# Kernel optimization log

Measured on AMD Instinct MI355X. Metric: run time of the kernel, lower is better.

Reference implementation:

```python
import jax, jax.numpy as jnp
import numpy as np

B, W, H = 128, 512, 512


def setup_inputs() -> dict:
    key = jax.random.key(0)
    ks = jax.random.split(key, 10)
    s = 1.0 / np.sqrt(H)
    return {
        "g": jax.random.normal(ks[0], (B, H), jnp.float32),
        "c_g": jax.random.normal(ks[1], (B, H), jnp.float32),
        "h": jax.random.normal(ks[2], (B, W, H), jnp.float32),
        "c": jax.random.normal(ks[3], (B, W, H), jnp.float32),
        "W_w": jax.random.normal(ks[4], (2 * H, H), jnp.float32) * s,
        "w_w": jax.random.normal(ks[5], (H, H), jnp.float32) * s,
        "U_w": jax.random.normal(ks[6], (2 * H, H), jnp.float32) * s,
        "U_b": jax.random.normal(ks[7], (2 * H,), jnp.float32) * s,
        "u_w": jax.random.normal(ks[8], (H, H), jnp.float32) * s,
        "u_b": jax.random.normal(ks[9], (H,), jnp.float32) * s,
    }


def reference(g, c_g, h, c, W_w, w_w, U_w, U_b, u_w, u_b):
    hid = w_w.shape[0]
    # attn_pooling: mean over word dim -> [B, H]
    h_avg = jnp.mean(h, axis=-2)
    # gates f, o: [B, H] each
    fo = jax.nn.sigmoid(g @ W_w.T + h_avg @ U_w.T + U_b)
    f, o = fo[..., :hid], fo[..., hid:]
    # per-word forget weights, softmax over word dim: [B, W, H]
    f_w = jax.nn.sigmoid((g @ w_w.T)[..., None, :] + h @ u_w.T + u_b)
    f_w = jax.nn.softmax(f_w, axis=-2)
    new_c = f * c_g + jnp.sum(c * f_w, axis=-2)
    new_g = o * jnp.tanh(new_c)
    return new_g, new_c
```

## Files before the change

kernel.cpp:

```cpp
#include <hip/hip_runtime.h>
#include <stdint.h>

#define BB 128
#define WW 512
#define HH 512
#define TILE 128
#define BK 64

typedef __attribute__((ext_vector_type(8))) short bf16x8;
typedef __attribute__((ext_vector_type(4))) float f32x4;

__device__ __forceinline__ float bf2f(unsigned short u) {
  union { unsigned int i; float f; } v;
  v.i = ((unsigned int)u) << 16;
  return v.f;
}
__device__ __forceinline__ unsigned int pack_bf2(float lo, float hi) {
  union { float f; unsigned int u; } a, b;
  a.f = lo; b.f = hi;
  return (a.u >> 16) | (b.u & 0xFFFF0000u);
}
__device__ __forceinline__ float dot4f(float4 u, const float* gp) {
  return u.x * gp[0] + u.y * gp[1] + u.z * gp[2] + u.w * gp[3];
}

__global__ __launch_bounds__(256) void k1_mfma(
    const float* __restrict__ g, const float* __restrict__ W_w,
    const float* __restrict__ w_w,
    float* __restrict__ gw, float* __restrict__ gfo) {
  __shared__ __align__(16) unsigned short As[TILE * BK];
  __shared__ __align__(16) unsigned short Bs[TILE * BK];
  const int nc = blockIdx.x;
  const int t = threadIdx.x;
  const int lane = t & 63, wave = t >> 6;
  const int wm = wave >> 1, wn = wave & 1;
  const int l15 = lane & 15, quad = lane >> 4;

  const float* wsrc = (nc < 4) ? (w_w + (size_t)nc * TILE * HH)
                               : (W_w + (size_t)(nc - 4) * TILE * HH);

  const f32x4 zero = {0.f, 0.f, 0.f, 0.f};
  f32x4 acc[4][4];
#pragma unroll
  for (int i = 0; i < 4; ++i)
#pragma unroll
    for (int j = 0; j < 4; ++j) acc[i][j] = zero;

  const int srow = t >> 3;
  const int scol = (t & 7) * 8;

  for (int kt = 0; kt < 8; ++kt) {
    const int k0 = kt * BK;
#pragma unroll
    for (int p = 0; p < 4; ++p) {
      const int row = p * 32 + srow;
      const float4* ap = (const float4*)(g    + (size_t)row * HH + k0 + scol);
      const float4* bp = (const float4*)(wsrc + (size_t)row * HH + k0 + scol);
      float4 a0 = ap[0], a1 = ap[1], b0 = bp[0], b1 = bp[1];
      uint4 av, bv;
      av.x = pack_bf2(a0.x, a0.y); av.y = pack_bf2(a0.z, a0.w);
      av.z = pack_bf2(a1.x, a1.y); av.w = pack_bf2(a1.z, a1.w);
      bv.x = pack_bf2(b0.x, b0.y); bv.y = pack_bf2(b0.z, b0.w);
      bv.z = pack_bf2(b1.x, b1.y); bv.w = pack_bf2(b1.z, b1.w);
      *(uint4*)(As + row * BK + scol) = av;
      *(uint4*)(Bs + row * BK + scol) = bv;
    }
    __syncthreads();
#pragma unroll
    for (int ks = 0; ks < 2; ++ks) {
      bf16x8 af[4], bg[4];
#pragma unroll
      for (int i = 0; i < 4; ++i)
        af[i] = *(const bf16x8*)(As + (wm * 64 + i * 16 + l15) * BK + ks * 32 + quad * 8);
#pragma unroll
      for (int j = 0; j < 4; ++j)
        bg[j] = *(const bf16x8*)(Bs + (wn * 64 + j * 16 + l15) * BK + ks * 32 + quad * 8);
#pragma unroll
      for (int i = 0; i < 4; ++i)
#pragma unroll
        for (int j = 0; j < 4; ++j)
          acc[i][j] = __builtin_amdgcn_mfma_f32_16x16x32_bf16(af[i], bg[j], acc[i][j], 0, 0, 0);
    }
    __syncthreads();
  }

#pragma unroll
  for (int j = 0; j < 4; ++j) {
    const int nl = wn * 64 + j * 16 + l15;
#pragma unroll
    for (int i = 0; i < 4; ++i) {
#pragma unroll
      for (int r = 0; r < 4; ++r) {
        const int b = wm * 64 + i * 16 + quad * 4 + r;
        const float v = acc[i][j][r];
        if (nc < 4) gw[(size_t)b * HH + nc * TILE + nl] = v;
        else        gfo[(size_t)b * 2 * HH + (nc - 4) * TILE + nl] = v;
      }
    }
  }
}

__global__ __launch_bounds__(256) void k2_main(
    const float* __restrict__ h, const float* __restrict__ c,
    const float* __restrict__ u_w, const float* __restrict__ u_b,
    const float* __restrict__ gw,
    float* __restrict__ hsumP, float* __restrict__ denP, float* __restrict__ numP) {
  __shared__ __align__(16) unsigned short As[TILE * BK];
  __shared__ __align__(16) unsigned short Bs[TILE * BK];
  __shared__ float colred[4][64];
  __shared__ float redD[2][TILE];
  __shared__ float redN[2][TILE];

  const int bid = blockIdx.x;
  const int b  = bid >> 4;
  const int wc = (bid >> 2) & 3;
  const int nc = bid & 3;
  const int t = threadIdx.x;
  const int lane = t & 63, wave = t >> 6;
  const int wm = wave >> 1, wn = wave & 1;
  const int l15 = lane & 15, quad = lane >> 4;

  const size_t hbase = ((size_t)b * WW + (size_t)wc * TILE) * HH;
  const size_t ubase = (size_t)nc * TILE * HH;

  const f32x4 zero = {0.f, 0.f, 0.f, 0.f};
  f32x4 acc[4][4];
#pragma unroll
  for (int i = 0; i < 4; ++i)
#pragma unroll
    for (int j = 0; j < 4; ++j) acc[i][j] = zero;

  const int srow = t >> 3;
  const int scol = (t & 7) * 8;

  for (int kt = 0; kt < 8; ++kt) {
    const int k0 = kt * BK;
#pragma unroll
    for (int p = 0; p < 4; ++p) {
      const int row = p * 32 + srow;
      const float4* ap = (const float4*)(h   + hbase + (size_t)row * HH + k0 + scol);
      const float4* bp = (const float4*)(u_w + ubase + (size_t)row * HH + k0 + scol);
      float4 a0 = ap[0], a1 = ap[1], b0 = bp[0], b1 = bp[1];
      uint4 av, bv;
      av.x = pack_bf2(a0.x, a0.y); av.y = pack_bf2(a0.z, a0.w);
      av.z = pack_bf2(a1.x, a1.y); av.w = pack_bf2(a1.z, a1.w);
      bv.x = pack_bf2(b0.x, b0.y); bv.y = pack_bf2(b0.z, b0.w);
      bv.z = pack_bf2(b1.x, b1.y); bv.w = pack_bf2(b1.z, b1.w);
      *(uint4*)(As + row * BK + scol) = av;
      *(uint4*)(Bs + row * BK + scol) = bv;
    }
    __syncthreads();

    if ((kt >> 1) == nc) {
      const int cidx = t & 63, mg = t >> 6;
      float s = 0.f;
#pragma unroll 8
      for (int m = mg * 32; m < mg * 32 + 32; ++m) s += bf2f(As[m * BK + cidx]);
      colred[mg][cidx] = s;
      __syncthreads();
      if (t < 64) {
        const float tot = colred[0][t] + colred[1][t] + colred[2][t] + colred[3][t];
        hsumP[((size_t)b * 4 + wc) * HH + nc * TILE + (kt & 1) * 64 + t] = tot;
      }
    }

#pragma unroll
    for (int ks = 0; ks < 2; ++ks) {
      bf16x8 af[4], bg[4];
#pragma unroll
      for (int i = 0; i < 4; ++i)
        af[i] = *(const bf16x8*)(As + (wm * 64 + i * 16 + l15) * BK + ks * 32 + quad * 8);
#pragma unroll
      for (int j = 0; j < 4; ++j)
        bg[j] = *(const bf16x8*)(Bs + (wn * 64 + j * 16 + l15) * BK + ks * 32 + quad * 8);
#pragma unroll
      for (int i = 0; i < 4; ++i)
#pragma unroll
        for (int j = 0; j < 4; ++j)
          acc[i][j] = __builtin_amdgcn_mfma_f32_16x16x32_bf16(af[i], bg[j], acc[i][j], 0, 0, 0);
    }
    __syncthreads();
  }

  const int N0 = nc * TILE;
#pragma unroll
  for (int j = 0; j < 4; ++j) {
    const int nl = wn * 64 + j * 16 + l15;
    const float gwub = gw[(size_t)b * HH + N0 + nl] + u_b[N0 + nl];
    float dsum = 0.f, nsum = 0.f;
#pragma unroll
    for (int i = 0; i < 4; ++i) {
#pragma unroll
      for (int r = 0; r < 4; ++r) {
        const int ml = wm * 64 + i * 16 + quad * 4 + r;
        const float z = acc[i][j][r] + gwub;
        const float sig = 1.f / (1.f + __expf(-z));
        const float e = __expf(sig);
        dsum += e;
        nsum += e * c[hbase + (size_t)ml * HH + N0 + nl];
      }
    }
    dsum += __shfl_xor(dsum, 16);
    dsum += __shfl_xor(dsum, 32);
    nsum += __shfl_xor(nsum, 16);
    nsum += __shfl_xor(nsum, 32);
    if (quad == 0) { redD[wm][nl] = dsum; redN[wm][nl] = nsum; }
  }
  __syncthreads();
  if (t < TILE) {
    const size_t o = ((size_t)b * 4 + wc) * HH + N0 + t;
    denP[o] = redD[0][t] + redD[1][t];
    numP[o] = redN[0][t] + redN[1][t];
  }
}

__global__ __launch_bounds__(256) void k3_final(
    const float* __restrict__ c_g, const float* __restrict__ U_w,
    const float* __restrict__ U_b,
    const float* __restrict__ gfo, const float* __restrict__ hsumP,
    const float* __restrict__ denP, const float* __restrict__ numP,
    float* __restrict__ out) {
  __shared__ float ha[HH];
  const int b = blockIdx.x, t = threadIdx.x;
  for (int i = t; i < HH; i += 256) {
    const float* hp = hsumP + (size_t)b * 4 * HH + i;
    ha[i] = (hp[0] + hp[HH] + hp[2 * HH] + hp[3 * HH]) * (1.f / (float)WW);
  }
  __syncthreads();
  for (int hh = 0; hh < 2; ++hh) {
    const int hid = hh * 256 + t;
    const float4* uf = (const float4*)(U_w + (size_t)hid * HH);
    const float4* uo = (const float4*)(U_w + (size_t)(HH + hid) * HH);
    float accf = 0.f, acco = 0.f;
    for (int k4 = 0; k4 < HH / 4; ++k4) {
      accf += dot4f(uf[k4], ha + k4 * 4);
      acco += dot4f(uo[k4], ha + k4 * 4);
    }
    const float flog = gfo[(size_t)b * 2 * HH + hid]      + accf + U_b[hid];
    const float olog = gfo[(size_t)b * 2 * HH + HH + hid] + acco + U_b[HH + hid];
    const float f = 1.f / (1.f + __expf(-flog));
    const float o = 1.f / (1.f + __expf(-olog));
    const float* dp = denP + (size_t)b * 4 * HH + hid;
    const float* np = numP + (size_t)b * 4 * HH + hid;
    const float den = dp[0] + dp[HH] + dp[2 * HH] + dp[3 * HH];
    const float num = np[0] + np[HH] + np[2 * HH] + np[3 * HH];
    const float ncv = f * c_g[(size_t)b * HH + hid] + num / den;
    const float ngv = o * tanhf(ncv);
    out[(size_t)b * HH + hid] = ngv;
    out[(size_t)BB * HH + (size_t)b * HH + hid] = ncv;
  }
}

extern "C" void kernel_launch(void* const* d_in, const int* in_sizes, int n_in,
                              void* d_out, int out_size, void* d_ws, size_t ws_size,
                              hipStream_t stream) {
  const float* g   = (const float*)d_in[0];
  const float* c_g = (const float*)d_in[1];
  const float* h   = (const float*)d_in[2];
  const float* c   = (const float*)d_in[3];
  const float* W_w = (const float*)d_in[4];
  const float* w_w = (const float*)d_in[5];
  const float* U_w = (const float*)d_in[6];
  const float* U_b = (const float*)d_in[7];
  const float* u_w = (const float*)d_in[8];
  const float* u_b = (const float*)d_in[9];

  float* ws    = (float*)d_ws;
  float* gw    = ws;
  float* gfo   = gw + BB * HH;
  float* hsumP = gfo + (size_t)BB * 2 * HH;
  float* denP  = hsumP + (size_t)BB * 4 * HH;
  float* numP  = denP + (size_t)BB * 4 * HH;
  float* out = (float*)d_out;

  hipLaunchKernelGGL(k1_mfma, dim3(12), dim3(256), 0, stream, g, W_w, w_w, gw, gfo);
  hipLaunchKernelGGL(k2_main, dim3(BB * 16), dim3(256), 0, stream,
                     h, c, u_w, u_b, gw, hsumP, denP, numP);
  hipLaunchKernelGGL(k3_final, dim3(BB), dim3(256), 0, stream,
                     c_g, U_w, U_b, gfo, hsumP, denP, numP, out);
}
```

Before: 439.9 us.

## Fuse N-tiles in main kernel, pre-convert u_w to swizzled bf16, split final kernel

The main kernel now has each 512-thread block cover all 512 output columns for one 128-word chunk. Each h tile is therefore loaded and converted to bf16 once instead of four times. u_w is pre-converted to a swizzled bf16 layout in the first kernel, and the main kernel streams it into LDS with global_load_lds. Shared-memory tiles use an XOR swizzle to avoid bank conflicts. The final kernel is split four ways per batch for more parallelism, at the cost of larger LDS and register use per block, which lowers occupancy.

After: 372.1 us. 1.18x faster.

```diff
diff --git a/kernel.cpp b/kernel.cpp
--- a/kernel.cpp
+++ b/kernel.cpp
@@ -23,15 +23,41 @@
 __device__ __forceinline__ float dot4f(float4 u, const float* gp) {
   return u.x * gp[0] + u.y * gp[1] + u.z * gp[2] + u.w * gp[3];
 }
-
-__global__ __launch_bounds__(256) void k1_mfma(
+__device__ __forceinline__ void gload_lds16(const void* src, void* lds_dst) {
+  __builtin_amdgcn_global_load_lds(
+      (const __attribute__((address_space(1))) unsigned int*)src,
+      (__attribute__((address_space(3))) unsigned int*)lds_dst, 16, 0, 0);
+}
+
+__global__ __launch_bounds__(256) void k01(
     const float* __restrict__ g, const float* __restrict__ W_w,
-    const float* __restrict__ w_w,
-    float* __restrict__ gw, float* __restrict__ gfo) {
+    const float* __restrict__ w_w, const float* __restrict__ u_w,
+    float* __restrict__ gw, float* __restrict__ gfo,
+    unsigned short* __restrict__ u_wb) {
   __shared__ __align__(16) unsigned short As[TILE * BK];
   __shared__ __align__(16) unsigned short Bs[TILE * BK];
-  const int nc = blockIdx.x;
+  const int bid = blockIdx.x;
   const int t = threadIdx.x;
+
+  if (bid >= 12) {
+    const int cid0 = (bid - 12) * 256 + t;
+    for (int idx = cid0; idx < 32768; idx += 16384) {
+      const int kt  = idx >> 12;
+      const int rem = idx & 4095;
+      const int r   = rem >> 3;
+      const int e   = (rem & 7) * 8;
+      const int c0  = kt * 64 + (e ^ ((r & 7) << 3));
+      const float4* sp = (const float4*)(u_w + (size_t)r * HH + c0);
+      float4 s0 = sp[0], s1 = sp[1];
+      uint4 pv;
+      pv.x = pack_bf2(s0.x, s0.y); pv.y = pack_bf2(s0.z, s0.w);
+      pv.z = pack_bf2(s1.x, s1.y); pv.w = pack_bf2(s1.z, s1.w);
+      *(uint4*)(u_wb + (size_t)idx * 8) = pv;
+    }
+    return;
+  }
+
+  const int nc = bid;
   const int lane = t & 63, wave = t >> 6;
   const int wm = wave >> 1, wn = wave & 1;
   const int l15 = lane & 15, quad = lane >> 4;
@@ -100,115 +126,132 @@
   }
 }
 
-__global__ __launch_bounds__(256) void k2_main(
+__global__ __launch_bounds__(512, 2) void k2_fused(
     const float* __restrict__ h, const float* __restrict__ c,
-    const float* __restrict__ u_w, const float* __restrict__ u_b,
+    const unsigned short* __restrict__ u_wb, const float* __restrict__ u_b,
     const float* __restrict__ gw,
     float* __restrict__ hsumP, float* __restrict__ denP, float* __restrict__ numP) {
-  __shared__ __align__(16) unsigned short As[TILE * BK];
-  __shared__ __align__(16) unsigned short Bs[TILE * BK];
-  __shared__ float colred[4][64];
-  __shared__ float redD[2][TILE];
-  __shared__ float redN[2][TILE];
+  __shared__ __align__(16) unsigned short Bs[512 * 64];
+  __shared__ __align__(16) unsigned short As[128 * 64];
+  __shared__ float colred[8][64];
+  __shared__ float redD[2][512];
+  __shared__ float redN[2][512];
 
   const int bid = blockIdx.x;
-  const int b  = bid >> 4;
-  const int wc = (bid >> 2) & 3;
-  const int nc = bid & 3;
+  const int b = bid >> 2, wc = bid & 3;
   const int t = threadIdx.x;
   const int lane = t & 63, wave = t >> 6;
-  const int wm = wave >> 1, wn = wave & 1;
+  const int wm = wave >> 2, wn = wave & 3;
   const int l15 = lane & 15, quad = lane >> 4;
 
-  const size_t hbase = ((size_t)b * WW + (size_t)wc * TILE) * HH;
-  const size_t ubase = (size_t)nc * TILE * HH;
+  const size_t hbase = ((size_t)b * WW + (size_t)wc * 128) * HH;
 
   const f32x4 zero = {0.f, 0.f, 0.f, 0.f};
-  f32x4 acc[4][4];
+  f32x4 acc[4][8];
 #pragma unroll
   for (int i = 0; i < 4; ++i)
 #pragma unroll
-    for (int j = 0; j < 4; ++j) acc[i][j] = zero;
+    for (int j = 0; j < 8; ++j) acc[i][j] = zero;
 
   const int srow = t >> 3;
   const int scol = (t & 7) * 8;
 
   for (int kt = 0; kt < 8; ++kt) {
-    const int k0 = kt * BK;
-#pragma unroll
-    for (int p = 0; p < 4; ++p) {
-      const int row = p * 32 + srow;
-      const float4* ap = (const float4*)(h   + hbase + (size_t)row * HH + k0 + scol);
-      const float4* bp = (const float4*)(u_w + ubase + (size_t)row * HH + k0 + scol);
-      float4 a0 = ap[0], a1 = ap[1], b0 = bp[0], b1 = bp[1];
-      uint4 av, bv;
+    const int k0 = kt * 64;
+
+    if (kt > 0 && t < 64) {
+      float tot = 0.f;
+#pragma unroll
+      for (int gq = 0; gq < 8; ++gq) tot += colred[gq][t];
+      hsumP[((size_t)b * 4 + wc) * HH + (kt - 1) * 64 + t] = tot;
+    }
+
+#pragma unroll
+    for (int it = 0; it < 8; ++it) {
+      const int s = wave * 8 + it;
+      const unsigned short* src =
+          u_wb + ((size_t)kt * 32768 + (size_t)s * 512 + (size_t)lane * 8);
+      gload_lds16(src, Bs + (size_t)s * 512);
+    }
+
+#pragma unroll
+    for (int p = 0; p < 2; ++p) {
+      const int row = p * 64 + srow;
+      const float4* ap = (const float4*)(h + hbase + (size_t)row * HH + k0 + scol);
+      float4 a0 = ap[0], a1 = ap[1];
+      uint4 av;
       av.x = pack_bf2(a0.x, a0.y); av.y = pack_bf2(a0.z, a0.w);
       av.z = pack_bf2(a1.x, a1.y); av.w = pack_bf2(a1.z, a1.w);
-      bv.x = pack_bf2(b0.x, b0.y); bv.y = pack_bf2(b0.z, b0.w);
-      bv.z = pack_bf2(b1.x, b1.y); bv.w = pack_bf2(b1.z, b1.w);
-      *(uint4*)(As + row * BK + scol) = av;
-      *(uint4*)(Bs + row * BK + scol) = bv;
+      *(uint4*)(As + row * 64 + (scol ^ ((row & 7) << 3))) = av;
     }
     __syncthreads();
 
-    if ((kt >> 1) == nc) {
-      const int cidx = t & 63, mg = t >> 6;
+    {
+      const int col = t & 63, gq = t >> 6;
       float s = 0.f;
-#pragma unroll 8
-      for (int m = mg * 32; m < mg * 32 + 32; ++m) s += bf2f(As[m * BK + cidx]);
-      colred[mg][cidx] = s;
-      __syncthreads();
-      if (t < 64) {
-        const float tot = colred[0][t] + colred[1][t] + colred[2][t] + colred[3][t];
-        hsumP[((size_t)b * 4 + wc) * HH + nc * TILE + (kt & 1) * 64 + t] = tot;
-      }
+#pragma unroll
+      for (int rr = 0; rr < 16; ++rr) {
+        const int row = gq * 16 + rr;
+        s += bf2f(As[row * 64 + (col ^ ((row & 7) << 3))]);
+      }
+      colred[gq][col] = s;
     }
 
 #pragma unroll
     for (int ks = 0; ks < 2; ++ks) {
-      bf16x8 af[4], bg[4];
+      bf16x8 af[4], bg[8];
+#pragma unroll
+      for (int i = 0; i < 4; ++i) {
+        const int row = wm * 64 + i * 16 + l15;
+        af[i] = *(const bf16x8*)(As + row * 64 + ((ks * 32 + quad * 8) ^ ((row & 7) << 3)));
+      }
+#pragma unroll
+      for (int j = 0; j < 8; ++j) {
+        const int row = wn * 128 + j * 16 + l15;
+        bg[j] = *(const bf16x8*)(Bs + row * 64 + ((ks * 32 + quad * 8) ^ ((row & 7) << 3)));
+      }
 #pragma unroll
       for (int i = 0; i < 4; ++i)
-        af[i] = *(const bf16x8*)(As + (wm * 64 + i * 16 + l15) * BK + ks * 32 + quad * 8);
-#pragma unroll
-      for (int j = 0; j < 4; ++j)
-        bg[j] = *(const bf16x8*)(Bs + (wn * 64 + j * 16 + l15) * BK + ks * 32 + quad * 8);
-#pragma unroll
-      for (int i = 0; i < 4; ++i)
-#pragma unroll
-        for (int j = 0; j < 4; ++j)
+#pragma unroll
+        for (int j = 0; j < 8; ++j)
           acc[i][j] = __builtin_amdgcn_mfma_f32_16x16x32_bf16(af[i], bg[j], acc[i][j], 0, 0, 0);
     }
     __syncthreads();
   }
 
-  const int N0 = nc * TILE;
-#pragma unroll
-  for (int j = 0; j < 4; ++j) {
-    const int nl = wn * 64 + j * 16 + l15;
-    const float gwub = gw[(size_t)b * HH + N0 + nl] + u_b[N0 + nl];
+  if (t < 64) {
+    float tot = 0.f;
+#pragma unroll
+    for (int gq = 0; gq < 8; ++gq) tot += colred[gq][t];
+    hsumP[((size_t)b * 4 + wc) * HH + 7 * 64 + t] = tot;
+  }
+
+#pragma unroll
+  for (int j = 0; j < 8; ++j) {
+    const int n = wn * 128 + j * 16 + l15;
+    const float gwub = gw[(size_t)b * HH + n] + u_b[n];
     float dsum = 0.f, nsum = 0.f;
 #pragma unroll
     for (int i = 0; i < 4; ++i) {
 #pragma unroll
       for (int r = 0; r < 4; ++r) {
-        const int ml = wm * 64 + i * 16 + quad * 4 + r;
+        const int m = wm * 64 + i * 16 + quad * 4 + r;
         const float z = acc[i][j][r] + gwub;
         const float sig = 1.f / (1.f + __expf(-z));
         const float e = __expf(sig);
         dsum += e;
-        nsum += e * c[hbase + (size_t)ml * HH + N0 + nl];
+        nsum += e * c[hbase + (size_t)m * HH + n];
       }
     }
     dsum += __shfl_xor(dsum, 16);
     dsum += __shfl_xor(dsum, 32);
     nsum += __shfl_xor(nsum, 16);
     nsum += __shfl_xor(nsum, 32);
-    if (quad == 0) { redD[wm][nl] = dsum; redN[wm][nl] = nsum; }
+    if (quad == 0) { redD[wm][n] = dsum; redN[wm][n] = nsum; }
   }
   __syncthreads();
-  if (t < TILE) {
-    const size_t o = ((size_t)b * 4 + wc) * HH + N0 + t;
+  {
+    const size_t o = ((size_t)b * 4 + wc) * HH + t;
     denP[o] = redD[0][t] + redD[1][t];
     numP[o] = redN[0][t] + redN[1][t];
   }
@@ -220,34 +263,50 @@
     const float* __restrict__ gfo, const float* __restrict__ hsumP,
     const float* __restrict__ denP, const float* __restrict__ numP,
     float* __restrict__ out) {
-  __shared__ float ha[HH];
-  const int b = blockIdx.x, t = threadIdx.x;
+  __shared__ __align__(16) float ha[HH];
+  __shared__ float ncL[128];
+  __shared__ float oL[128];
+  const int bid = blockIdx.x;
+  const int b = bid >> 2, q = bid & 3;
+  const int t = threadIdx.x;
+
   for (int i = t; i < HH; i += 256) {
     const float* hp = hsumP + (size_t)b * 4 * HH + i;
     ha[i] = (hp[0] + hp[HH] + hp[2 * HH] + hp[3 * HH]) * (1.f / (float)WW);
   }
   __syncthreads();
-  for (int hh = 0; hh < 2; ++hh) {
-    const int hid = hh * 256 + t;
-    const float4* uf = (const float4*)(U_w + (size_t)hid * HH);
-    const float4* uo = (const float4*)(U_w + (size_t)(HH + hid) * HH);
-    float accf = 0.f, acco = 0.f;
-    for (int k4 = 0; k4 < HH / 4; ++k4) {
-      accf += dot4f(uf[k4], ha + k4 * 4);
-      acco += dot4f(uo[k4], ha + k4 * 4);
-    }
-    const float flog = gfo[(size_t)b * 2 * HH + hid]      + accf + U_b[hid];
-    const float olog = gfo[(size_t)b * 2 * HH + HH + hid] + acco + U_b[HH + hid];
-    const float f = 1.f / (1.f + __expf(-flog));
-    const float o = 1.f / (1.f + __expf(-olog));
-    const float* dp = denP + (size_t)b * 4 * HH + hid;
-    const float* np = numP + (size_t)b * 4 * HH + hid;
+
+  const int isF = (t < 128);
+  const int n = q * 128 + (t & 127);
+  const int row = isF ? n : (HH + n);
+  const float4* up = (const float4*)(U_w + (size_t)row * HH);
+
+  float p0 = 0.f, p1 = 0.f, p2 = 0.f, p3 = 0.f;
+#pragma unroll 4
+  for (int k4 = 0; k4 < 128; k4 += 4) {
+    p0 += dot4f(up[k4 + 0], ha + k4 * 4 + 0);
+    p1 += dot4f(up[k4 + 1], ha + k4 * 4 + 4);
+    p2 += dot4f(up[k4 + 2], ha + k4 * 4 + 8);
+    p3 += dot4f(up[k4 + 3], ha + k4 * 4 + 12);
+  }
+  const float dot = (p0 + p1) + (p2 + p3);
+  const float logit = gfo[(size_t)b * 2 * HH + row] + dot + U_b[row];
+  const float sg = 1.f / (1.f + __expf(-logit));
+
+  if (isF) {
+    const float* dp = denP + (size_t)b * 4 * HH + n;
+    const float* np = numP + (size_t)b * 4 * HH + n;
     const float den = dp[0] + dp[HH] + dp[2 * HH] + dp[3 * HH];
     const float num = np[0] + np[HH] + np[2 * HH] + np[3 * HH];
-    const float ncv = f * c_g[(size_t)b * HH + hid] + num / den;
-    const float ngv = o * tanhf(ncv);
-    out[(size_t)b * HH + hid] = ngv;
-    out[(size_t)BB * HH + (size_t)b * HH + hid] = ncv;
+    const float ncv = sg * c_g[(size_t)b * HH + n] + num / den;
+    ncL[t] = ncv;
+    out[(size_t)BB * HH + (size_t)b * HH + n] = ncv;
+  } else {
+    oL[t - 128] = sg;
+  }
+  __syncthreads();
+  if (isF) {
+    out[(size_t)b * HH + n] = oL[t] * tanhf(ncL[t]);
   }
 }
 
@@ -271,11 +330,12 @@
   float* hsumP = gfo + (size_t)BB * 2 * HH;
   float* denP  = hsumP + (size_t)BB * 4 * HH;
   float* numP  = denP + (size_t)BB * 4 * HH;
+  unsigned short* u_wb = (unsigned short*)(numP + (size_t)BB * 4 * HH);
   float* out = (float*)d_out;
 
-  hipLaunchKernelGGL(k1_mfma, dim3(12), dim3(256), 0, stream, g, W_w, w_w, gw, gfo);
-  hipLaunchKernelGGL(k2_main, dim3(BB * 16), dim3(256), 0, stream,
-                     h, c, u_w, u_b, gw, hsumP, denP, numP);
-  hipLaunchKernelGGL(k3_final, dim3(BB), dim3(256), 0, stream,
+  hipLaunchKernelGGL(k01, dim3(76), dim3(256), 0, stream, g, W_w, w_w, u_w, gw, gfo, u_wb);
+  hipLaunchKernelGGL(k2_fused, dim3(512), dim3(512), 0, stream,
+                     h, c, u_wb, u_b, gw, hsumP, denP, numP);
+  hipLaunchKernelGGL(k3_final, dim3(512), dim3(256), 0, stream,
                      c_g, U_w, U_b, gfo, hsumP, denP, numP, out);
 }
```
